# Optimization experiments

Measured on AMD Instinct MI355X. Metric: run time of the kernel, lower is better.

## Reference

```python
import jax, jax.numpy as jnp
import numpy as np

N_HEAD = 16
WINDOW = 256
GLOBAL = 32


def _sparse_mask(T):
    # local window of +/- WINDOW//2 plus global rows/cols for first GLOBAL tokens
    i = jnp.arange(T)
    local = jnp.abs(i[:, None] - i[None, :]) <= (WINDOW // 2)
    glob = (i[:, None] < GLOBAL) | (i[None, :] < GLOBAL)
    return local | glob  # [T, T] bool


def setup_inputs() -> dict:
    key = jax.random.key(0)
    k1, k2, k3 = jax.random.split(key, 3)
    B, T, C = 1, 4096, 1024
    scale = 0.02
    return {
        "x": jax.random.normal(k1, (B, T, C), dtype=jnp.float32),
        "W_attn": jax.random.normal(k2, (C, 3 * C), dtype=jnp.float32) * scale,
        "b_attn": jnp.zeros((3 * C,), dtype=jnp.float32),
        "W_proj": jax.random.normal(k3, (C, C), dtype=jnp.float32) * scale,
        "b_proj": jnp.zeros((C,), dtype=jnp.float32),
    }


def reference(x, W_attn, b_attn, W_proj, b_proj):
    B, T, C = x.shape
    H = N_HEAD
    D = C // H

    qkv = x @ W_attn + b_attn  # [B, T, 3C]
    q, k, v = jnp.split(qkv, 3, axis=-1)
    # [B, H, T, D]
    q = q.reshape(B, T, H, D).transpose(0, 2, 1, 3)
    k = k.reshape(B, T, H, D).transpose(0, 2, 1, 3)
    v = v.reshape(B, T, H, D).transpose(0, 2, 1, 3)

    mask = _sparse_mask(T)  # [T, T]
    att = jnp.einsum("bhqd,bhkd->bhqk", q, k) * (1.0 / np.sqrt(D))
    neg = jnp.finfo(att.dtype).min
    att = jnp.where(mask, att, neg)
    att = jax.nn.softmax(att, axis=-1)
    y = jnp.einsum("bhqk,bhkd->bhqd", att, v)  # [B, H, T, D]
    y = y.transpose(0, 2, 1, 3).reshape(B, T, C)
    return y @ W_proj + b_proj
```

## Files before the change

kernel.cpp:

```cpp
#include <hip/hip_runtime.h>
#include <hip/hip_bf16.h>
#include <math.h>

#define T_SEQ 4096
#define C_DIM 1024
#define H_HEADS 16
#define D_HEAD 64
#define QKVW 3072
#define WIN_HALF 128
#define GLOBAL_TOK 32

typedef __attribute__((ext_vector_type(8))) short bf16x8;
typedef __attribute__((ext_vector_type(4))) float f32x4;

__device__ __forceinline__ float bf2f(unsigned short u) {
    union { unsigned int i; float f; } c; c.i = ((unsigned int)u) << 16; return c.f;
}
__device__ __forceinline__ unsigned short f2bf(float f) {
    union { float f; unsigned int i; } c; c.f = f;
    return (unsigned short)((c.i + 0x7fffu + ((c.i >> 16) & 1u)) >> 16);
}

__device__ __forceinline__ void gll16(const unsigned short* g, unsigned short* l) {
    __builtin_amdgcn_global_load_lds(
        (const __attribute__((address_space(1))) void*)g,
        (__attribute__((address_space(3))) void*)l, 16, 0, 0);
}

__device__ __forceinline__ int swz(int row, int chunk) {
    return row * 64 + ((chunk ^ (row & 7)) * 8);
}

__global__ __launch_bounds__(256) void cvt_f32_bf16_kernel(
    const float* __restrict__ src, unsigned short* __restrict__ dst, int n4)
{
    int idx = blockIdx.x * 256 + threadIdx.x;
    if (idx < n4) {
        float4 v = ((const float4*)src)[idx];
        ushort4 o;
        o.x = f2bf(v.x); o.y = f2bf(v.y); o.z = f2bf(v.z); o.w = f2bf(v.w);
        ((ushort4*)dst)[idx] = o;
    }
}

__global__ __launch_bounds__(256) void cvt_transpose_kernel(
    const float* __restrict__ src, unsigned short* __restrict__ dst,
    int R, int Ncols)
{
    __shared__ unsigned short tile[32][36];
    const int r0 = blockIdx.y * 32, c0 = blockIdx.x * 32;
    const int t = threadIdx.x;
    const int rr = t >> 3, cq = (t & 7) * 4;
    float4 v = *(const float4*)(src + (size_t)(r0 + rr) * Ncols + c0 + cq);
    tile[rr][cq + 0] = f2bf(v.x); tile[rr][cq + 1] = f2bf(v.y);
    tile[rr][cq + 2] = f2bf(v.z); tile[rr][cq + 3] = f2bf(v.w);
    __syncthreads();
    const int cc = t >> 3, rq = (t & 7) * 4;
    ushort4 o;
    o.x = tile[rq + 0][cc]; o.y = tile[rq + 1][cc];
    o.z = tile[rq + 2][cc]; o.w = tile[rq + 3][cc];
    *(ushort4*)(dst + (size_t)(c0 + cc) * R + r0 + rq) = o;
}

__global__ __launch_bounds__(256) void transpose_v_kernel(
    const unsigned short* __restrict__ qkv, unsigned short* __restrict__ vT)
{
    __shared__ unsigned short tile[32][36];
    const int c0 = blockIdx.x * 32;
    const int t0 = blockIdx.y * 32;
    const int t = threadIdx.x;
    const int rr = t >> 3, cq = (t & 7) * 4;
    ushort4 v = *(const ushort4*)(qkv + (size_t)(t0 + rr) * QKVW + 2 * C_DIM + c0 + cq);
    tile[rr][cq + 0] = v.x; tile[rr][cq + 1] = v.y;
    tile[rr][cq + 2] = v.z; tile[rr][cq + 3] = v.w;
    __syncthreads();
    const int cc = t >> 3, rq = (t & 7) * 4;
    ushort4 o;
    o.x = tile[rq + 0][cc]; o.y = tile[rq + 1][cc];
    o.z = tile[rq + 2][cc]; o.w = tile[rq + 3][cc];
    *(ushort4*)(vT + (size_t)(c0 + cc) * T_SEQ + t0 + rq) = o;
}

template<int OUT_BF16>
__global__ __launch_bounds__(256) void gemm_nt_kernel(
    const unsigned short* __restrict__ A,
    const unsigned short* __restrict__ Bt,
    const float* __restrict__ bias,
    void* __restrict__ Cv, int M, int N, int K)
{
    __shared__ unsigned short As[128 * 32];
    __shared__ unsigned short Bs[128 * 32];
    const int tid = threadIdx.x;
    const int w = tid >> 6, lane = tid & 63;
    const int quad = lane >> 4, r16 = lane & 15;
    const int m0 = blockIdx.y * 128, n0 = blockIdx.x * 128;
    const int wm = (w & 1) * 64, wn = (w >> 1) * 64;

    f32x4 acc[4][4];
    #pragma unroll
    for (int i = 0; i < 4; ++i)
        #pragma unroll
        for (int j = 0; j < 4; ++j) acc[i][j] = (f32x4){0.f, 0.f, 0.f, 0.f};

    const unsigned short* Ab = A + (size_t)m0 * K;
    const unsigned short* Bb = Bt + (size_t)n0 * K;

    for (int k0 = 0; k0 < K; k0 += 32) {
        __syncthreads();
        #pragma unroll
        for (int i = 0; i < 2; ++i) {
            const int chunk = w * 128 + i * 64 + lane;
            const int row = chunk >> 2, kc = (chunk & 3) * 8;
            gll16(Ab + (size_t)row * K + k0 + kc, &As[(w * 2 + i) * 512]);
            gll16(Bb + (size_t)row * K + k0 + kc, &Bs[(w * 2 + i) * 512]);
        }
        asm volatile("s_waitcnt vmcnt(0)" ::: "memory");
        __builtin_amdgcn_sched_barrier(0);
        __syncthreads();

        bf16x8 af[4], bf_[4];
        #pragma unroll
        for (int t = 0; t < 4; ++t) {
            af[t]  = *(const bf16x8*)&As[(wm + t * 16 + r16) * 32 + quad * 8];
            bf_[t] = *(const bf16x8*)&Bs[(wn + t * 16 + r16) * 32 + quad * 8];
        }
        #pragma unroll
        for (int mt = 0; mt < 4; ++mt)
            #pragma unroll
            for (int nt = 0; nt < 4; ++nt)
                acc[mt][nt] = __builtin_amdgcn_mfma_f32_16x16x32_bf16(
                    af[mt], bf_[nt], acc[mt][nt], 0, 0, 0);
    }

    #pragma unroll
    for (int nt = 0; nt < 4; ++nt) {
        const int col = n0 + wn + nt * 16 + r16;
        const float bv = bias[col];
        #pragma unroll
        for (int mt = 0; mt < 4; ++mt)
            #pragma unroll
            for (int reg = 0; reg < 4; ++reg) {
                const int row = m0 + wm + mt * 16 + quad * 4 + reg;
                if (OUT_BF16)
                    ((unsigned short*)Cv)[(size_t)row * N + col] = f2bf(acc[mt][nt][reg] + bv);
                else
                    ((float*)Cv)[(size_t)row * N + col] = acc[mt][nt][reg] + bv;
            }
    }
}

#define PT_STRIDE 72
#define NSLOT 8
#define PROW 72

struct KVbuf { bf16x8 kl[4], kh[4], vl[4], vh[4]; };
struct StReg { bf16x8 a, b, c, d; };

#define LOAD_KV(C0, B)                                                         \
  {                                                                            \
    const unsigned short* kr_ = kb + (size_t)((C0) + n) * QKVW + quad * 8;     \
    _Pragma("unroll")                                                          \
    for (int g = 0; g < 4; ++g) {                                              \
      B.kl[g] = *(const bf16x8*)(kr_ + (size_t)(g * 16) * QKVW);               \
      B.kh[g] = *(const bf16x8*)(kr_ + (size_t)(g * 16) * QKVW + 32);          \
    }                                                                          \
    const unsigned short* vr_ = vb + (size_t)n * T_SEQ + (C0) + quad * 8;      \
    _Pragma("unroll")                                                          \
    for (int d = 0; d < 4; ++d) {                                              \
      B.vl[d] = *(const bf16x8*)(vr_ + (size_t)(d * 16) * T_SEQ);              \
      B.vh[d] = *(const bf16x8*)(vr_ + (size_t)(d * 16) * T_SEQ + 32);         \
    }                                                                          \
  }

#define SOFTMAX_P_UPDATE(StV)                                                  \
    mm = fmaxf(mm, __shfl_xor(mm, 16));                                        \
    mm = fmaxf(mm, __shfl_xor(mm, 32));                                        \
    const float mn = fmaxf(m_run, mm);                                         \
    const float mnf = (mn == -INFINITY) ? 0.f : mn;                            \
    const float al = __expf(m_run - mnf);                                      \
    float rs = 0.f;                                                            \
    _Pragma("unroll")                                                          \
    for (int g = 0; g < 4; ++g) {                                              \
      const float e0 = __expf(StV[g][0] - mnf);                                \
      const float e1 = __expf(StV[g][1] - mnf);                                \
      const float e2 = __expf(StV[g][2] - mnf);                                \
      const float e3 = __expf(StV[g][3] - mnf);                                \
      rs += (e0 + e1) + (e2 + e3);                                             \
      const unsigned int p01 = f2bf(e0) | ((unsigned int)f2bf(e1) << 16);      \
      const unsigned int p23 = f2bf(e2) | ((unsigned int)f2bf(e3) << 16);      \
      *(unsigned int*)&myPt[n * PT_STRIDE + g * 16 + quad * 4] = p01;          \
      *(unsigned int*)&myPt[n * PT_STRIDE + g * 16 + quad * 4 + 2] = p23;      \
    }                                                                          \
    rs += __shfl_xor(rs, 16);                                                  \
    rs += __shfl_xor(rs, 32);                                                  \
    l_run = l_run * al + rs;                                                   \
    m_run = mn;                                                                \
    _Pragma("unroll")                                                          \
    for (int d = 0; d < 4; ++d)                                                \
      _Pragma("unroll")                                                        \
      for (int r = 0; r < 4; ++r) O[d][r] *= al;

#define PROC_TILE(ITV, CUR, NXT)                                               \
  {                                                                            \
    const int it_ = (ITV);                                                     \
    const int c0 = split * 512 + it_ * 64;                                     \
    f32x4 St[4];                                                               \
    _Pragma("unroll")                                                          \
    for (int g = 0; g < 4; ++g) {                                              \
      St[g] = __builtin_amdgcn_mfma_f32_16x16x32_bf16(CUR.kl[g], q0, Zf, 0, 0, 0); \
      St[g] = __builtin_amdgcn_mfma_f32_16x16x32_bf16(CUR.kh[g], q1, St[g], 0, 0, 0); \
    }                                                                          \
    if (it_ + 1 < n_tiles) {                                                   \
      LOAD_KV(c0 + 64, NXT);                                                   \
    }                                                                          \
    float mm = -INFINITY;                                                      \
    _Pragma("unroll")                                                          \
    for (int g = 0; g < 4; ++g)                                                \
      _Pragma("unroll")                                                        \
      for (int r = 0; r < 4; ++r) {                                            \
        const float v = St[g][r] * 0.125f;                                     \
        St[g][r] = v; mm = fmaxf(mm, v);                                       \
      }                                                                        \
    SOFTMAX_P_UPDATE(St)                                                       \
    asm volatile("s_waitcnt lgkmcnt(0)" ::: "memory");                         \
    __builtin_amdgcn_sched_barrier(0);                                         \
    _Pragma("unroll")                                                          \
    for (int kg = 0; kg < 2; ++kg) {                                           \
      bf16x8 pf_ = *(const bf16x8*)&myPt[n * PT_STRIDE + kg * 32 + quad * 8];  \
      _Pragma("unroll")                                                        \
      for (int d = 0; d < 4; ++d)                                              \
        O[d] = __builtin_amdgcn_mfma_f32_16x16x32_bf16(                        \
            kg ? CUR.vh[d] : CUR.vl[d], pf_, O[d], 0, 0, 0);                   \
    }                                                                          \
  }

#define STAGE_LOAD(C0, R)                                                      \
  { const int c0s_ = (C0);                                                     \
    R.a = *(const bf16x8*)(kb + (size_t)(c0s_ + srow) * QKVW + scol * 8);      \
    R.b = *(const bf16x8*)(kb + (size_t)(c0s_ + srow + 32) * QKVW + scol * 8); \
    R.c = *(const bf16x8*)(vb + (size_t)srow * T_SEQ + c0s_ + scol * 8);       \
    R.d = *(const bf16x8*)(vb + (size_t)(srow + 32) * T_SEQ + c0s_ + scol * 8); }

#define STAGE_WRITE(BUF, R)                                                    \
  { *(bf16x8*)&Ks[BUF][kdst0] = R.a;                                           \
    *(bf16x8*)&Ks[BUF][kdst1] = R.b;                                           \
    *(bf16x8*)&Vs[BUF][kdst0] = R.c;                                           \
    *(bf16x8*)&Vs[BUF][kdst1] = R.d; }

#define WTILE(ITV, BUF, RW, RL)                                                \
  {                                                                            \
    const int it_ = (ITV);                                                     \
    const int c0 = (it_ == 0) ? 0 : (blo + (it_ - 1) * 64);                    \
    if (activeW) {                                                             \
      bf16x8 kl[4], kh[4];                                                     \
      _Pragma("unroll")                                                        \
      for (int g = 0; g < 4; ++g) {                                            \
        kl[g] = *(const bf16x8*)&Ks[BUF][swz(n + g * 16, quad)];               \
        kh[g] = *(const bf16x8*)&Ks[BUF][swz(n + g * 16, quad + 4)];           \
      }                                                                        \
      f32x4 St[4];                                                             \
      _Pragma("unroll")                                                        \
      for (int g = 0; g < 4; ++g) {                                            \
        St[g] = __builtin_amdgcn_mfma_f32_16x16x32_bf16(kl[g], q0, Zf, 0, 0, 0); \
        St[g] = __builtin_amdgcn_mfma_f32_16x16x32_bf16(kh[g], q1, St[g], 0, 0, 0); \
      }                                                                        \
      float mm = -INFINITY;                                                    \
      if (it_ != 0 && c0 >= rowbase - 113 && c0 <= rowbase + 65) {             \
        _Pragma("unroll")                                                      \
        for (int g = 0; g < 4; ++g)                                            \
          _Pragma("unroll")                                                    \
          for (int r = 0; r < 4; ++r) {                                        \
            const float v = St[g][r] * 0.125f;                                 \
            St[g][r] = v; mm = fmaxf(mm, v);                                   \
          }                                                                    \
      } else if (it_ == 0 && rowbase >= 192) {                                 \
        _Pragma("unroll")                                                      \
        for (int g = 0; g < 2; ++g)                                            \
          _Pragma("unroll")                                                    \
          for (int r = 0; r < 4; ++r) {                                        \
            const float v = St[g][r] * 0.125f;                                 \
            St[g][r] = v; mm = fmaxf(mm, v);                                   \
          }                                                                    \
        _Pragma("unroll")                                                      \
        for (int g = 2; g < 4; ++g)                                            \
          _Pragma("unroll")                                                    \
          for (int r = 0; r < 4; ++r) St[g][r] = -INFINITY;                    \
      } else {                                                                 \
        _Pragma("unroll")                                                      \
        for (int g = 0; g < 4; ++g)                                            \
          _Pragma("unroll")                                                    \
          for (int r = 0; r < 4; ++r) {                                        \
            float v = St[g][r] * 0.125f;                                       \
            const int col = c0 + g * 16 + quad * 4 + r;                        \
            int dd = row - col; dd = dd < 0 ? -dd : dd;                        \
            if (!(col < GLOBAL_TOK || dd <= WIN_HALF)) v = -INFINITY;          \
            St[g][r] = v; mm = fmaxf(mm, v);                                   \
          }                                                                    \
      }                                                                        \
      SOFTMAX_P_UPDATE(St)                                                     \
      bf16x8 vl[4], vh[4];                                                     \
      _Pragma("unroll")                                                        \
      for (int d = 0; d < 4; ++d) {                                            \
        vl[d] = *(const bf16x8*)&Vs[BUF][swz(n + d * 16, quad)];               \
        vh[d] = *(const bf16x8*)&Vs[BUF][swz(n + d * 16, quad + 4)];           \
      }                                                                        \
      asm volatile("s_waitcnt lgkmcnt(0)" ::: "memory");                       \
      __builtin_amdgcn_sched_barrier(0);                                       \
      _Pragma("unroll")                                                        \
      for (int kg = 0; kg < 2; ++kg) {                                         \
        bf16x8 pf_ = *(const bf16x8*)&myPt[n * PT_STRIDE + kg * 32 + quad * 8];\
        _Pragma("unroll")                                                      \
        for (int d = 0; d < 4; ++d)                                            \
          O[d] = __builtin_amdgcn_mfma_f32_16x16x32_bf16(                      \
              kg ? vh[d] : vl[d], pf_, O[d], 0, 0, 0);                         \
      }                                                                        \
    }                                                                          \
    if (it_ + 1 < NT) {                                                        \
      asm volatile("s_waitcnt vmcnt(0)" ::: "memory");                         \
      __builtin_amdgcn_sched_barrier(0);                                       \
      STAGE_WRITE((BUF) ^ 1, RW);                                              \
      if (it_ + 2 < NT) { STAGE_LOAD(blo + (it_ + 1) * 64, RL); }              \
      __syncthreads();                                                         \
    }                                                                          \
  }

__global__ __launch_bounds__(256, 3) void sparse_attn_mfma(
    const unsigned short* __restrict__ qkv,
    const unsigned short* __restrict__ vT,
    unsigned short* __restrict__ y,
    float* __restrict__ part)
{
    __shared__ unsigned short Ks[2][64 * 64];
    __shared__ unsigned short Vs[2][64 * 64];
    __shared__ unsigned short Pt[4][16 * PT_STRIDE];
    const int tid = threadIdx.x;
    const int w = tid >> 6, lane = tid & 63;
    const int quad = lane >> 4, n = lane & 15;
    const int bid = blockIdx.x;
    const f32x4 Zf = (f32x4){0.f, 0.f, 0.f, 0.f};

    if (bid < 1024) {
        const int h = bid & 15;
        const int B = bid >> 4;
        const int base = B * 64;
        const int rowbase = base + w * 16;
        const bool activeW = !(B == 0 && w < 2);
        int blo = base - 128; if (blo < 64) blo = 64;
        int bhi = base + 192; if (bhi > T_SEQ) bhi = T_SEQ;
        const int NT = 1 + (bhi - blo) / 64;

        const unsigned short* kb = qkv + C_DIM + h * 64;
        const unsigned short* vb = vT + (size_t)h * 64 * T_SEQ;
        unsigned short* myPt = Pt[w];

        const int srow = tid >> 3, scol = tid & 7;
        const int kdst0 = swz(srow, scol);
        const int kdst1 = kdst0 + 32 * 64;

        const unsigned short* qp = qkv + (size_t)(rowbase + n) * QKVW + h * 64 + quad * 8;
        bf16x8 q0 = *(const bf16x8*)qp;
        bf16x8 q1 = *(const bf16x8*)(qp + 32);

        f32x4 O[4];
        #pragma unroll
        for (int i = 0; i < 4; ++i) O[i] = (f32x4){0.f, 0.f, 0.f, 0.f};
        float m_run = -INFINITY, l_run = 0.f;
        const int row = rowbase + n;

        StReg r0, r1;
        STAGE_LOAD(0, r0);
        asm volatile("s_waitcnt vmcnt(0)" ::: "memory");
        __builtin_amdgcn_sched_barrier(0);
        STAGE_WRITE(0, r0);
        STAGE_LOAD(blo, r1);
        __syncthreads();

        int it = 0;
        for (;;) {
            WTILE(it, 0, r1, r0);
            if (++it >= NT) break;
            WTILE(it, 1, r0, r1);
            if (++it >= NT) break;
        }

        if (activeW) {
            const float invL = 1.f / l_run;
            #pragma unroll
            for (int dblk = 0; dblk < 4; ++dblk)
                #pragma unroll
                for (int r = 0; r < 4; ++r)
                    y[(size_t)row * C_DIM + h * 64 + dblk * 16 + quad * 4 + r] =
                        f2bf(O[dblk][r] * invL);
        }
    } else {
        const int idx = bid - 1024;
        const int h = idx & 15;
        const int u = (idx >> 4) * 4 + w;
        const int rt = u >> 3, split = u & 7;
        const int rowbase = rt * 16;
        const int n_tiles = 8;

        const unsigned short* qp = qkv + (size_t)(rowbase + n) * QKVW + h * 64 + quad * 8;
        bf16x8 q0 = *(const bf16x8*)qp;
        bf16x8 q1 = *(const bf16x8*)(qp + 32);

        const unsigned short* kb = qkv + C_DIM + h * 64;
        const unsigned short* vb = vT + (size_t)h * 64 * T_SEQ;
        unsigned short* myPt = Pt[w];

        f32x4 O[4];
        #pragma unroll
        for (int i = 0; i < 4; ++i) O[i] = (f32x4){0.f, 0.f, 0.f, 0.f};
        float m_run = -INFINITY, l_run = 0.f;

        KVbuf b0, b1;
        LOAD_KV(split * 512, b0);
        int it = 0;
        for (;;) {
            PROC_TILE(it, b0, b1);
            if (++it >= n_tiles) break;
            PROC_TILE(it, b1, b0);
            if (++it >= n_tiles) break;
        }

        float* pb = part + ((size_t)(h * 2 + rt) * NSLOT + split) * 16 * PROW;
        #pragma unroll
        for (int dblk = 0; dblk < 4; ++dblk)
            #pragma unroll
            for (int r = 0; r < 4; ++r)
                pb[n * PROW + dblk * 16 + quad * 4 + r] = O[dblk][r];
        if (quad == 0) {
            pb[n * PROW + 64] = m_run;
            pb[n * PROW + 65] = l_run;
        }
    }
}

__global__ __launch_bounds__(64) void attn_combine(
    const float* __restrict__ part, unsigned short* __restrict__ y)
{
    const int d = threadIdx.x;
    const int h = blockIdx.x >> 1, rt = blockIdx.x & 1;
    const float* base = part + (size_t)(h * 2 + rt) * NSLOT * 16 * PROW;
    for (int row = 0; row < 16; ++row) {
        float M = -INFINITY;
        for (int sl = 0; sl < NSLOT; ++sl)
            M = fmaxf(M, base[(size_t)sl * 16 * PROW + row * PROW + 64]);
        float L = 0.f, Od = 0.f;
        for (int sl = 0; sl < NSLOT; ++sl) {
            const float* p = base + (size_t)sl * 16 * PROW + row * PROW;
            const float s = __expf(p[64] - M);
            L += p[65] * s;
            Od += p[d] * s;
        }
        y[(size_t)(rt * 16 + row) * C_DIM + h * 64 + d] = f2bf(Od / L);
    }
}

extern "C" void kernel_launch(void* const* d_in, const int* in_sizes, int n_in,
                              void* d_out, int out_size, void* d_ws, size_t ws_size,
                              hipStream_t stream) {
    const float* x  = (const float*)d_in[0];
    const float* Wa = (const float*)d_in[1];
    const float* ba = (const float*)d_in[2];
    const float* Wp = (const float*)d_in[3];
    const float* bp = (const float*)d_in[4];
    float* out = (float*)d_out;

    unsigned short* xb   = (unsigned short*)d_ws;
    unsigned short* Wabt = xb   + (size_t)T_SEQ * C_DIM;
    unsigned short* Wpbt = Wabt + (size_t)C_DIM * QKVW;
    unsigned short* qkv  = Wpbt + (size_t)C_DIM * C_DIM;
    unsigned short* yat  = qkv  + (size_t)T_SEQ * QKVW;
    unsigned short* vT = xb;
    float* part = (float*)Wabt;

    const int n_x = T_SEQ * C_DIM;
    cvt_f32_bf16_kernel<<<n_x / 4 / 256, 256, 0, stream>>>(x, xb, n_x / 4);
    cvt_transpose_kernel<<<dim3(QKVW / 32, C_DIM / 32), 256, 0, stream>>>(
        Wa, Wabt, C_DIM, QKVW);
    cvt_transpose_kernel<<<dim3(C_DIM / 32, C_DIM / 32), 256, 0, stream>>>(
        Wp, Wpbt, C_DIM, C_DIM);

    gemm_nt_kernel<1><<<dim3(QKVW / 128, T_SEQ / 128), 256, 0, stream>>>(
        xb, Wabt, ba, qkv, T_SEQ, QKVW, C_DIM);

    transpose_v_kernel<<<dim3(C_DIM / 32, T_SEQ / 32), 256, 0, stream>>>(qkv, vT);

    const int nBlocks = 1024 + 64;
    sparse_attn_mfma<<<nBlocks, 256, 0, stream>>>(qkv, vT, yat, part);
    attn_combine<<<H_HEADS * 2, 64, 0, stream>>>(part, yat);

    gemm_nt_kernel<0><<<dim3(C_DIM / 128, T_SEQ / 128), 256, 0, stream>>>(
        yat, Wpbt, bp, out, T_SEQ, C_DIM, C_DIM);
}
```

Before: 201.0 us.

## Fuse prep conversions, write V transposed from QKV GEMM, remap blocks, add setprio

```diff
diff --git a/kernel.cpp b/kernel.cpp
--- a/kernel.cpp
+++ b/kernel.cpp
@@ -31,25 +31,34 @@
     return row * 64 + ((chunk ^ (row & 7)) * 8);
 }
 
-__global__ __launch_bounds__(256) void cvt_f32_bf16_kernel(
-    const float* __restrict__ src, unsigned short* __restrict__ dst, int n4)
+__global__ __launch_bounds__(256) void prep_kernel(
+    const float* __restrict__ x, const float* __restrict__ Wa,
+    const float* __restrict__ Wp,
+    unsigned short* __restrict__ xb, unsigned short* __restrict__ Wabt,
+    unsigned short* __restrict__ Wpbt)
 {
-    int idx = blockIdx.x * 256 + threadIdx.x;
-    if (idx < n4) {
-        float4 v = ((const float4*)src)[idx];
+    __shared__ unsigned short tile[32][36];
+    const int bid = blockIdx.x;
+    const int t = threadIdx.x;
+    if (bid < 4096) {
+        const int idx = bid * 256 + t;
+        float4 v = ((const float4*)x)[idx];
         ushort4 o;
         o.x = f2bf(v.x); o.y = f2bf(v.y); o.z = f2bf(v.z); o.w = f2bf(v.w);
-        ((ushort4*)dst)[idx] = o;
+        ((ushort4*)xb)[idx] = o;
+        return;
     }
-}
-
-__global__ __launch_bounds__(256) void cvt_transpose_kernel(
-    const float* __restrict__ src, unsigned short* __restrict__ dst,
-    int R, int Ncols)
-{
-    __shared__ unsigned short tile[32][36];
-    const int r0 = blockIdx.y * 32, c0 = blockIdx.x * 32;
-    const int t = threadIdx.x;
+    const float* src; unsigned short* dst; int R, Ncols, bx, by;
+    if (bid < 4096 + 3072) {
+        const int b = bid - 4096;
+        src = Wa; dst = Wabt; R = C_DIM; Ncols = QKVW;
+        bx = b % (QKVW / 32); by = b / (QKVW / 32);
+    } else {
+        const int b = bid - 7168;
+        src = Wp; dst = Wpbt; R = C_DIM; Ncols = C_DIM;
+        bx = b % (C_DIM / 32); by = b / (C_DIM / 32);
+    }
+    const int r0 = by * 32, c0 = bx * 32;
     const int rr = t >> 3, cq = (t & 7) * 4;
     float4 v = *(const float4*)(src + (size_t)(r0 + rr) * Ncols + c0 + cq);
     tile[rr][cq + 0] = f2bf(v.x); tile[rr][cq + 1] = f2bf(v.y);
@@ -62,38 +71,24 @@
     *(ushort4*)(dst + (size_t)(c0 + cc) * R + r0 + rq) = o;
 }
 
-__global__ __launch_bounds__(256) void transpose_v_kernel(
-    const unsigned short* __restrict__ qkv, unsigned short* __restrict__ vT)
-{
-    __shared__ unsigned short tile[32][36];
-    const int c0 = blockIdx.x * 32;
-    const int t0 = blockIdx.y * 32;
-    const int t = threadIdx.x;
-    const int rr = t >> 3, cq = (t & 7) * 4;
-    ushort4 v = *(const ushort4*)(qkv + (size_t)(t0 + rr) * QKVW + 2 * C_DIM + c0 + cq);
-    tile[rr][cq + 0] = v.x; tile[rr][cq + 1] = v.y;
-    tile[rr][cq + 2] = v.z; tile[rr][cq + 3] = v.w;
-    __syncthreads();
-    const int cc = t >> 3, rq = (t & 7) * 4;
-    ushort4 o;
-    o.x = tile[rq + 0][cc]; o.y = tile[rq + 1][cc];
-    o.z = tile[rq + 2][cc]; o.w = tile[rq + 3][cc];
-    *(ushort4*)(vT + (size_t)(c0 + cc) * T_SEQ + t0 + rq) = o;
-}
-
-template<int OUT_BF16>
+template<int OUT_BF16, int WRITE_VT>
 __global__ __launch_bounds__(256) void gemm_nt_kernel(
     const unsigned short* __restrict__ A,
     const unsigned short* __restrict__ Bt,
     const float* __restrict__ bias,
-    void* __restrict__ Cv, int M, int N, int K)
+    void* __restrict__ Cv, unsigned short* __restrict__ vTp,
+    int M, int N, int K)
 {
     __shared__ unsigned short As[128 * 32];
     __shared__ unsigned short Bs[128 * 32];
     const int tid = threadIdx.x;
     const int w = tid >> 6, lane = tid & 63;
     const int quad = lane >> 4, r16 = lane & 15;
-    const int m0 = blockIdx.y * 128, n0 = blockIdx.x * 128;
+    const int nbx = gridDim.x;
+    const int nwg = nbx * gridDim.y;
+    int lb = blockIdx.y * nbx + blockIdx.x;
+    lb = (lb & 7) * (nwg >> 3) + (lb >> 3);
+    const int m0 = (lb / nbx) * 128, n0 = (lb % nbx) * 128;
     const int wm = (w & 1) * 64, wn = (w >> 1) * 64;
 
     f32x4 acc[4][4];
@@ -132,20 +127,38 @@
                     af[mt], bf_[nt], acc[mt][nt], 0, 0, 0);
     }
 
-    #pragma unroll
-    for (int nt = 0; nt < 4; ++nt) {
-        const int col = n0 + wn + nt * 16 + r16;
-        const float bv = bias[col];
-        #pragma unroll
-        for (int mt = 0; mt < 4; ++mt)
+    if (WRITE_VT && n0 >= 2 * C_DIM) {
+        #pragma unroll
+        for (int nt = 0; nt < 4; ++nt) {
+            const int col = n0 + wn + nt * 16 + r16;
+            const float bv = bias[col];
+            const int vcol = col - 2 * C_DIM;
             #pragma unroll
-            for (int reg = 0; reg < 4; ++reg) {
-                const int row = m0 + wm + mt * 16 + quad * 4 + reg;
-                if (OUT_BF16)
-                    ((unsigned short*)Cv)[(size_t)row * N + col] = f2bf(acc[mt][nt][reg] + bv);
-                else
-                    ((float*)Cv)[(size_t)row * N + col] = acc[mt][nt][reg] + bv;
+            for (int mt = 0; mt < 4; ++mt) {
+                ushort4 o;
+                o.x = f2bf(acc[mt][nt][0] + bv);
+                o.y = f2bf(acc[mt][nt][1] + bv);
+                o.z = f2bf(acc[mt][nt][2] + bv);
+                o.w = f2bf(acc[mt][nt][3] + bv);
+                *(ushort4*)&vTp[(size_t)vcol * T_SEQ + m0 + wm + mt * 16 + quad * 4] = o;
             }
+        }
+    } else {
+        #pragma unroll
+        for (int nt = 0; nt < 4; ++nt) {
+            const int col = n0 + wn + nt * 16 + r16;
+            const float bv = bias[col];
+            #pragma unroll
+            for (int mt = 0; mt < 4; ++mt)
+                #pragma unroll
+                for (int reg = 0; reg < 4; ++reg) {
+                    const int row = m0 + wm + mt * 16 + quad * 4 + reg;
+                    if (OUT_BF16)
+                        ((unsigned short*)Cv)[(size_t)row * N + col] = f2bf(acc[mt][nt][reg] + bv);
+                    else
+                        ((float*)Cv)[(size_t)row * N + col] = acc[mt][nt][reg] + bv;
+                }
+        }
     }
 }
 
@@ -205,11 +218,13 @@
     const int it_ = (ITV);                                                     \
     const int c0 = split * 512 + it_ * 64;                                     \
     f32x4 St[4];                                                               \
+    __builtin_amdgcn_s_setprio(1);                                             \
     _Pragma("unroll")                                                          \
     for (int g = 0; g < 4; ++g) {                                              \
       St[g] = __builtin_amdgcn_mfma_f32_16x16x32_bf16(CUR.kl[g], q0, Zf, 0, 0, 0); \
       St[g] = __builtin_amdgcn_mfma_f32_16x16x32_bf16(CUR.kh[g], q1, St[g], 0, 0, 0); \
     }                                                                          \
+    __builtin_amdgcn_s_setprio(0);                                             \
     if (it_ + 1 < n_tiles) {                                                   \
       LOAD_KV(c0 + 64, NXT);                                                   \
     }                                                                          \
@@ -224,6 +239,7 @@
     SOFTMAX_P_UPDATE(St)                                                       \
     asm volatile("s_waitcnt lgkmcnt(0)" ::: "memory");                         \
     __builtin_amdgcn_sched_barrier(0);                                         \
+    __builtin_amdgcn_s_setprio(1);                                             \
     _Pragma("unroll")                                                          \
     for (int kg = 0; kg < 2; ++kg) {                                           \
       bf16x8 pf_ = *(const bf16x8*)&myPt[n * PT_STRIDE + kg * 32 + quad * 8];  \
@@ -232,6 +248,7 @@
         O[d] = __builtin_amdgcn_mfma_f32_16x16x32_bf16(                        \
             kg ? CUR.vh[d] : CUR.vl[d], pf_, O[d], 0, 0, 0);                   \
     }                                                                          \
+    __builtin_amdgcn_s_setprio(0);                                             \
   }
 
 #define STAGE_LOAD(C0, R)                                                      \
@@ -259,11 +276,13 @@
         kh[g] = *(const bf16x8*)&Ks[BUF][swz(n + g * 16, quad + 4)];           \
       }                                                                        \
       f32x4 St[4];                                                             \
+      __builtin_amdgcn_s_setprio(1);                                           \
       _Pragma("unroll")                                                        \
       for (int g = 0; g < 4; ++g) {                                            \
         St[g] = __builtin_amdgcn_mfma_f32_16x16x32_bf16(kl[g], q0, Zf, 0, 0, 0); \
         St[g] = __builtin_amdgcn_mfma_f32_16x16x32_bf16(kh[g], q1, St[g], 0, 0, 0); \
       }                                                                        \
+      __builtin_amdgcn_s_setprio(0);                                           \
       float mm = -INFINITY;                                                    \
       if (it_ != 0 && c0 >= rowbase - 113 && c0 <= rowbase + 65) {             \
         _Pragma("unroll")                                                      \
@@ -306,6 +325,7 @@
       }                                                                        \
       asm volatile("s_waitcnt lgkmcnt(0)" ::: "memory");                       \
       __builtin_amdgcn_sched_barrier(0);                                       \
+      __builtin_amdgcn_s_setprio(1);                                           \
       _Pragma("unroll")                                                        \
       for (int kg = 0; kg < 2; ++kg) {                                         \
         bf16x8 pf_ = *(const bf16x8*)&myPt[n * PT_STRIDE + kg * 32 + quad * 8];\
@@ -314,6 +334,7 @@
           O[d] = __builtin_amdgcn_mfma_f32_16x16x32_bf16(                      \
               kg ? vh[d] : vl[d], pf_, O[d], 0, 0, 0);                         \
       }                                                                        \
+      __builtin_amdgcn_s_setprio(0);                                           \
     }                                                                          \
     if (it_ + 1 < NT) {                                                        \
       asm volatile("s_waitcnt vmcnt(0)" ::: "memory");                         \
@@ -472,25 +493,19 @@
     unsigned short* Wpbt = Wabt + (size_t)C_DIM * QKVW;
     unsigned short* qkv  = Wpbt + (size_t)C_DIM * C_DIM;
     unsigned short* yat  = qkv  + (size_t)T_SEQ * QKVW;
-    unsigned short* vT = xb;
-    float* part = (float*)Wabt;
-
-    const int n_x = T_SEQ * C_DIM;
-    cvt_f32_bf16_kernel<<<n_x / 4 / 256, 256, 0, stream>>>(x, xb, n_x / 4);
-    cvt_transpose_kernel<<<dim3(QKVW / 32, C_DIM / 32), 256, 0, stream>>>(
-        Wa, Wabt, C_DIM, QKVW);
-    cvt_transpose_kernel<<<dim3(C_DIM / 32, C_DIM / 32), 256, 0, stream>>>(
-        Wp, Wpbt, C_DIM, C_DIM);
-
-    gemm_nt_kernel<1><<<dim3(QKVW / 128, T_SEQ / 128), 256, 0, stream>>>(
-        xb, Wabt, ba, qkv, T_SEQ, QKVW, C_DIM);
-
-    transpose_v_kernel<<<dim3(C_DIM / 32, T_SEQ / 32), 256, 0, stream>>>(qkv, vT);
+    unsigned short* vT   = yat  + (size_t)T_SEQ * C_DIM;
+    float* part = (float*)(vT + (size_t)C_DIM * T_SEQ);
+
+    prep_kernel<<<4096 + 3072 + 1024, 256, 0, stream>>>(
+        x, Wa, Wp, xb, Wabt, Wpbt);
+
+    gemm_nt_kernel<1, 1><<<dim3(QKVW / 128, T_SEQ / 128), 256, 0, stream>>>(
+        xb, Wabt, ba, qkv, vT, T_SEQ, QKVW, C_DIM);
 
     const int nBlocks = 1024 + 64;
     sparse_attn_mfma<<<nBlocks, 256, 0, stream>>>(qkv, vT, yat, part);
     attn_combine<<<H_HEADS * 2, 64, 0, stream>>>(part, yat);
 
-    gemm_nt_kernel<0><<<dim3(C_DIM / 128, T_SEQ / 128), 256, 0, stream>>>(
-        yat, Wpbt, bp, out, T_SEQ, C_DIM, C_DIM);
-}
+    gemm_nt_kernel<0, 0><<<dim3(C_DIM / 128, T_SEQ / 128), 256, 0, stream>>>(
+        yat, Wpbt, bp, out, nullptr, T_SEQ, C_DIM, C_DIM);
+}
```

After: 206.7 us. +2.9%, slower.
